# Performance work log

Measured on AMD Instinct MI355X. Metric: run time of the kernel, lower is better.

Reference implementation:

```python
import jax, jax.numpy as jnp
import numpy as np

N_NODES = 20000
N_EDGES = 200000
NODE_DIM = 32
EDGE_DIM = 16
HIDDEN = 32
N_GRAPHS = 64


def setup_inputs() -> dict:
    key = jax.random.key(0)
    ks = jax.random.split(key, 20)
    x = jax.random.normal(ks[0], (N_NODES, NODE_DIM), jnp.float32)
    edge_attr = jax.random.normal(ks[1], (N_EDGES, EDGE_DIM), jnp.float32)
    edge_index = jax.random.randint(ks[2], (2, N_EDGES), 0, N_NODES, jnp.int64)
    batch = jnp.sort(jax.random.randint(ks[3], (N_NODES,), 0, N_GRAPHS, jnp.int64))
    s = 0.1
    # conv1 edge network: EDGE_DIM -> HIDDEN -> NODE_DIM*HIDDEN
    en1_W1 = jax.random.normal(ks[4], (EDGE_DIM, HIDDEN), jnp.float32) * s
    en1_b1 = jnp.zeros((HIDDEN,), jnp.float32)
    en1_W2 = jax.random.normal(ks[5], (HIDDEN, NODE_DIM * HIDDEN), jnp.float32) * s
    en1_b2 = jnp.zeros((NODE_DIM * HIDDEN,), jnp.float32)
    root1 = jax.random.normal(ks[6], (NODE_DIM, HIDDEN), jnp.float32) * s
    bias1 = jnp.zeros((HIDDEN,), jnp.float32)
    # conv2 edge network: EDGE_DIM -> HIDDEN -> HIDDEN*HIDDEN
    en2_W1 = jax.random.normal(ks[7], (EDGE_DIM, HIDDEN), jnp.float32) * s
    en2_b1 = jnp.zeros((HIDDEN,), jnp.float32)
    en2_W2 = jax.random.normal(ks[8], (HIDDEN, HIDDEN * HIDDEN), jnp.float32) * s
    en2_b2 = jnp.zeros((HIDDEN * HIDDEN,), jnp.float32)
    root2 = jax.random.normal(ks[9], (HIDDEN, HIDDEN), jnp.float32) * s
    bias2 = jnp.zeros((HIDDEN,), jnp.float32)
    # output head
    fc_W = jax.random.normal(ks[10], (HIDDEN, 2), jnp.float32) * s
    fc_b = jnp.zeros((2,), jnp.float32)
    return {
        "x": x, "edge_attr": edge_attr, "edge_index": edge_index, "batch": batch,
        "en1_W1": en1_W1, "en1_b1": en1_b1, "en1_W2": en1_W2, "en1_b2": en1_b2,
        "root1": root1, "bias1": bias1,
        "en2_W1": en2_W1, "en2_b1": en2_b1, "en2_W2": en2_W2, "en2_b2": en2_b2,
        "root2": root2, "bias2": bias2,
        "fc_W": fc_W, "fc_b": fc_b,
    }


def _segment_mean(vals, ids, num_segments):
    s = jax.ops.segment_sum(vals, ids, num_segments=num_segments)
    cnt = jax.ops.segment_sum(jnp.ones((vals.shape[0],), vals.dtype), ids, num_segments=num_segments)
    return s / jnp.maximum(cnt, 1.0)[:, None]


def _nnconv(x, src, tgt, edge_attr, W1, b1, W2, b2, root, bias, in_c, out_c, n_nodes):
    # edge MLP -> per-edge weight matrix [E, in_c, out_c]
    h = jax.nn.relu(edge_attr @ W1 + b1)
    Wedge = (h @ W2 + b2).reshape(-1, in_c, out_c)
    # gather source feats, per-edge matvec, scatter-mean to targets
    msg = jnp.einsum('ei,eio->eo', x[src], Wedge)
    agg = _segment_mean(msg, tgt, n_nodes)
    return agg + x @ root + bias


def reference(x, edge_attr, edge_index, batch,
              en1_W1, en1_b1, en1_W2, en1_b2, root1, bias1,
              en2_W1, en2_b1, en2_W2, en2_b2, root2, bias2,
              fc_W, fc_b):
    src, tgt = edge_index[0], edge_index[1]
    h = _nnconv(x, src, tgt, edge_attr, en1_W1, en1_b1, en1_W2, en1_b2,
                root1, bias1, NODE_DIM, HIDDEN, N_NODES)
    h = jax.nn.relu(h)
    h = _nnconv(h, src, tgt, edge_attr, en2_W1, en2_b1, en2_W2, en2_b2,
                root2, bias2, HIDDEN, HIDDEN, N_NODES)
    h = jax.nn.relu(h)
    g = _segment_mean(h, batch, N_GRAPHS)  # global_mean_pool
    return g @ fc_W + fc_b
```

## Files before the change

kernel.cpp:

```cpp
#include <hip/hip_runtime.h>

#define N_NODES   20000
#define N_EDGES   200000
#define NODE_DIM  32
#define EDGE_DIM  16
#define HIDDEN    32
#define N_GRAPHS  64
#define T_NODES   15


__global__ __launch_bounds__(256) void build_deg2_kernel(
    const int* __restrict__ tgts, const int* __restrict__ srcs,
    int* __restrict__ deg_t, int* __restrict__ deg_s)
{
    int e = blockIdx.x * blockDim.x + threadIdx.x;
    if (e >= N_EDGES) return;
    atomicAdd(deg_t + tgts[e], 1);
    atomicAdd(deg_s + srcs[e], 1);
}

__device__ void chunked_scan(const int* __restrict__ deg, int* __restrict__ start,
                             int* __restrict__ cursor, int* partial)
{
    const int C = (N_NODES + 255) / 256;
    int t  = threadIdx.x;
    int lo = t * C;
    int hi = lo + C < N_NODES ? lo + C : N_NODES;
    int s = 0;
    for (int i = lo; i < hi; ++i) s += deg[i];
    partial[t] = s;
    __syncthreads();
    if (t == 0) {
        int run = 0;
        for (int i = 0; i < 256; ++i) { int v = partial[i]; partial[i] = run; run += v; }
    }
    __syncthreads();
    int run = partial[t];
    for (int i = lo; i < hi; ++i) {
        start[i]  = run;
        cursor[i] = run;
        run += deg[i];
    }
    if (lo < N_NODES && hi == N_NODES) start[N_NODES] = run;
    __syncthreads();
}

__global__ __launch_bounds__(256) void scan2_kernel(
    const int* __restrict__ deg_t, int* __restrict__ start_t, int* __restrict__ cur_t,
    const int* __restrict__ deg_s, int* __restrict__ start_s, int* __restrict__ cur_s)
{
    __shared__ int partial[256];
    chunked_scan(deg_t, start_t, cur_t, partial);
    chunked_scan(deg_s, start_s, cur_s, partial);
}

__global__ __launch_bounds__(256) void scatter2_kernel(
    const int* __restrict__ tgts, const int* __restrict__ srcs,
    int* __restrict__ cur_t, int* __restrict__ cur_s,
    int* __restrict__ pos_t, int* __restrict__ eid_s)
{
    int e = blockIdx.x * blockDim.x + threadIdx.x;
    if (e >= N_EDGES) return;
    int p1 = atomicAdd(cur_t + tgts[e], 1);
    pos_t[e] = p1;
    int p2 = atomicAdd(cur_s + srcs[e], 1);
    eid_s[p2] = e;
}

__global__ __launch_bounds__(256, 2) void src_conv_kernel(
    const float* __restrict__ feat,
    const float* __restrict__ ea,
    const int*   __restrict__ srcs,
    const int*   __restrict__ start_s,
    const int*   __restrict__ eid_s,
    const int*   __restrict__ pos_t,
    const float* __restrict__ W1,
    const float* __restrict__ b1,
    const float* __restrict__ W2,
    const float* __restrict__ b2,
    float*       __restrict__ msg)
{
    __shared__ float P[T_NODES][32][32];
    __shared__ float Q[T_NODES][32];
    __shared__ float XT[T_NODES][32];

    int tid = threadIdx.x;
    int v0  = blockIdx.x * T_NODES;
    int T_act = (N_NODES - v0) < T_NODES ? (N_NODES - v0) : T_NODES;

    if (tid < 8 * T_NODES) {
        int t  = tid >> 3;
        int og = tid & 7;
        int vv = v0 + t; if (vv > N_NODES - 1) vv = N_NODES - 1;
        float4 xx = *reinterpret_cast<const float4*>(feat + (size_t)vv * 32 + og * 4);
        *reinterpret_cast<float4*>(&XT[t][og * 4]) = xx;
    }
    __syncthreads();

    {
        int og = tid & 7;
        int k  = tid >> 3;
        float acc[T_NODES][4];
        #pragma unroll
        for (int t = 0; t < T_NODES; ++t) {
            acc[t][0] = 0.f; acc[t][1] = 0.f; acc[t][2] = 0.f; acc[t][3] = 0.f;
        }
        const float* w2p = W2 + (size_t)k * 1024 + og * 4;
        #pragma unroll
        for (int i = 0; i < 32; ++i) {
            float4 w4 = *reinterpret_cast<const float4*>(w2p + i * 32);
            #pragma unroll
            for (int t = 0; t < T_NODES; ++t) {
                float xv = XT[t][i];
                acc[t][0] += xv * w4.x; acc[t][1] += xv * w4.y;
                acc[t][2] += xv * w4.z; acc[t][3] += xv * w4.w;
            }
        }
        #pragma unroll
        for (int t = 0; t < T_NODES; ++t) {
            float4 w; w.x = acc[t][0]; w.y = acc[t][1]; w.z = acc[t][2]; w.w = acc[t][3];
            *reinterpret_cast<float4*>(&P[t][k][og * 4]) = w;
        }
    }
    if (tid < 8 * T_NODES) {
        int t  = tid >> 3;
        int og = tid & 7;
        float q0 = 0.f, q1 = 0.f, q2 = 0.f, q3 = 0.f;
        const float* b2p = b2 + og * 4;
        #pragma unroll
        for (int i = 0; i < 32; ++i) {
            float4 b4 = *reinterpret_cast<const float4*>(b2p + i * 32);
            float xv = XT[t][i];
            q0 += xv * b4.x; q1 += xv * b4.y; q2 += xv * b4.z; q3 += xv * b4.w;
        }
        float4 qq; qq.x = q0; qq.y = q1; qq.z = q2; qq.w = q3;
        *reinterpret_cast<float4*>(&Q[t][og * 4]) = qq;
    }
    __syncthreads();

    int jb = start_s[v0];
    int je = start_s[v0 + T_act];
    int slot = tid >> 5;
    int kl   = tid & 31;
    int half = tid & 32;

    float w1c[EDGE_DIM];
    #pragma unroll
    for (int j = 0; j < EDGE_DIM; ++j) w1c[j] = W1[j * 32 + kl];
    float b1v = b1[kl];

    for (int j0 = jb; j0 < je; j0 += 8) {
        int j = j0 + slot;
        if (j < je) {
            int e  = eid_s[j];
            int sl = srcs[e] - v0;
            int pr = pos_t[e];
            const float4* ea4 = reinterpret_cast<const float4*>(ea + (size_t)e * EDGE_DIM);
            float4 a0 = ea4[0], a1 = ea4[1], a2 = ea4[2], a3 = ea4[3];
            float hv = b1v;
            hv += a0.x * w1c[0]  + a0.y * w1c[1]  + a0.z * w1c[2]  + a0.w * w1c[3];
            hv += a1.x * w1c[4]  + a1.y * w1c[5]  + a1.z * w1c[6]  + a1.w * w1c[7];
            hv += a2.x * w1c[8]  + a2.y * w1c[9]  + a2.z * w1c[10] + a2.w * w1c[11];
            hv += a3.x * w1c[12] + a3.y * w1c[13] + a3.z * w1c[14] + a3.w * w1c[15];
            float h = fmaxf(hv, 0.f);

            float accv = Q[sl][kl];
            #pragma unroll
            for (int k = 0; k < 32; ++k) {
                float hk = __shfl(h, half + k, 64);
                accv += hk * P[sl][k][kl];
            }
            msg[(size_t)pr * 32 + kl] = accv;
        }
    }
}

__global__ __launch_bounds__(256) void gather_update_kernel(
    const float* __restrict__ feat,
    const float* __restrict__ msg,
    const int*   __restrict__ start,
    const float* __restrict__ root,
    const float* __restrict__ bias,
    float*       __restrict__ outf,
    const int*   __restrict__ batch,
    float*       __restrict__ pool,
    float*       __restrict__ pcnt)
{
    int idx = blockIdx.x * blockDim.x + threadIdx.x;
    int v = idx >> 5;
    int o = idx & 31;
    if (v >= N_NODES) return;

    int s0 = start[v], s1 = start[v + 1];
    float sum = 0.0f;
    int j = s0;
    for (; j + 4 <= s1; j += 4) {
        float m0 = msg[(size_t)(j + 0) * 32 + o];
        float m1 = msg[(size_t)(j + 1) * 32 + o];
        float m2 = msg[(size_t)(j + 2) * 32 + o];
        float m3 = msg[(size_t)(j + 3) * 32 + o];
        sum += (m0 + m1) + (m2 + m3);
    }
    for (; j < s1; ++j) sum += msg[(size_t)j * 32 + o];

    int d = s1 - s0;
    float acc = sum / (float)(d > 0 ? d : 1) + bias[o];

    const float* xv = feat + (size_t)v * 32;
    #pragma unroll
    for (int i = 0; i < 32; ++i) acc += xv[i] * root[i * 32 + o];
    acc = fmaxf(acc, 0.0f);

    if (outf) outf[(size_t)v * 32 + o] = acc;
    if (batch) {
        int g = batch[v];
        atomicAdd(pool + (size_t)g * 32 + o, acc);
        if (o == 0) atomicAdd(pcnt + g, 1.0f);
    }
}

__global__ void head_kernel(
    const float* __restrict__ pool, const float* __restrict__ pcnt,
    const float* __restrict__ fcW, const float* __restrict__ fcb,
    float* __restrict__ out)
{
    int g = threadIdx.x;
    if (g >= N_GRAPHS) return;
    float inv = 1.0f / fmaxf(pcnt[g], 1.0f);
    float o0 = fcb[0], o1 = fcb[1];
    #pragma unroll
    for (int i = 0; i < 32; ++i) {
        float m = pool[g * 32 + i] * inv;
        o0 += m * fcW[i * 2 + 0];
        o1 += m * fcW[i * 2 + 1];
    }
    out[g * 2 + 0] = o0;
    out[g * 2 + 1] = o1;
}

__global__ __launch_bounds__(256) void build_deg_kernel(
    const int* __restrict__ tgts, int* __restrict__ deg)
{
    int e = blockIdx.x * blockDim.x + threadIdx.x;
    if (e >= N_EDGES) return;
    atomicAdd(deg + tgts[e], 1);
}

__global__ __launch_bounds__(256) void scan_deg_kernel(
    const int* __restrict__ deg, int* __restrict__ start, int* __restrict__ cursor)
{
    __shared__ int partial[256];
    chunked_scan(deg, start, cursor, partial);
}

__global__ __launch_bounds__(256) void scatter_edges_kernel(
    const int* __restrict__ tgts, int* __restrict__ cursor, int* __restrict__ eid)
{
    int e = blockIdx.x * blockDim.x + threadIdx.x;
    if (e >= N_EDGES) return;
    int pos = atomicAdd(cursor + tgts[e], 1);
    eid[pos] = e;
}

__global__ __launch_bounds__(256) void edge_msg_kernel(
    const float* __restrict__ feat, const float* __restrict__ ea,
    const int* __restrict__ srcs,
    const float* __restrict__ W1, const float* __restrict__ b1,
    const float* __restrict__ W2, const float* __restrict__ b2,
    float* __restrict__ msg)
{
    int e = blockIdx.x * blockDim.x + threadIdx.x;
    if (e >= N_EDGES) return;
    float a[EDGE_DIM];
    const float4* ea4 = reinterpret_cast<const float4*>(ea + (size_t)e * EDGE_DIM);
    #pragma unroll
    for (int q = 0; q < EDGE_DIM / 4; ++q) {
        float4 t = ea4[q];
        a[q*4+0] = t.x; a[q*4+1] = t.y; a[q*4+2] = t.z; a[q*4+3] = t.w;
    }
    int s = srcs[e];
    float x[32];
    const float4* x4 = reinterpret_cast<const float4*>(feat + (size_t)s * 32);
    #pragma unroll
    for (int q = 0; q < 8; ++q) {
        float4 t = x4[q];
        x[q*4+0] = t.x; x[q*4+1] = t.y; x[q*4+2] = t.z; x[q*4+3] = t.w;
    }
    float acc[32];
    #pragma unroll
    for (int o = 0; o < 32; ++o) acc[o] = 0.0f;
    #pragma unroll
    for (int i = 0; i < 32; ++i) {
        float xi = x[i];
        #pragma unroll
        for (int o = 0; o < 32; ++o) acc[o] += xi * b2[i*32+o];
    }
    for (int k = 0; k < 32; ++k) {
        float hk = b1[k];
        #pragma unroll
        for (int j = 0; j < EDGE_DIM; ++j) hk += a[j] * W1[j*32 + k];
        hk = fmaxf(hk, 0.0f);
        const float* w = W2 + (size_t)k * 1024;
        #pragma unroll
        for (int i = 0; i < 32; ++i) {
            float c = hk * x[i];
            #pragma unroll
            for (int o = 0; o < 32; ++o) acc[o] += c * w[i*32+o];
        }
    }
    float4* m4 = reinterpret_cast<float4*>(msg + (size_t)e * 32);
    #pragma unroll
    for (int q = 0; q < 8; ++q) {
        float4 t;
        t.x = acc[q*4+0]; t.y = acc[q*4+1]; t.z = acc[q*4+2]; t.w = acc[q*4+3];
        m4[q] = t;
    }
}

__global__ __launch_bounds__(256) void gather_update_eid_kernel(
    const float* __restrict__ feat, const float* __restrict__ msg,
    const int* __restrict__ start, const int* __restrict__ eid,
    const float* __restrict__ root, const float* __restrict__ bias,
    float* __restrict__ outf, const int* __restrict__ batch,
    float* __restrict__ pool, float* __restrict__ pcnt)
{
    int idx = blockIdx.x * blockDim.x + threadIdx.x;
    int v = idx >> 5;
    int o = idx & 31;
    if (v >= N_NODES) return;
    int s0 = start[v], s1 = start[v + 1];
    float sum = 0.0f;
    for (int j = s0; j < s1; ++j) {
        int e = eid[j];
        sum += msg[(size_t)e * 32 + o];
    }
    int d = s1 - s0;
    float acc = sum / (float)(d > 0 ? d : 1) + bias[o];
    const float* xv = feat + (size_t)v * 32;
    #pragma unroll
    for (int i = 0; i < 32; ++i) acc += xv[i] * root[i * 32 + o];
    acc = fmaxf(acc, 0.0f);
    if (outf) outf[(size_t)v * 32 + o] = acc;
    if (batch) {
        int g = batch[v];
        atomicAdd(pool + (size_t)g * 32 + o, acc);
        if (o == 0) atomicAdd(pcnt + g, 1.0f);
    }
}


extern "C" void kernel_launch(void* const* d_in, const int* in_sizes, int n_in,
                              void* d_out, int out_size, void* d_ws, size_t ws_size,
                              hipStream_t stream)
{
    const float* x      = (const float*)d_in[0];
    const float* ea     = (const float*)d_in[1];
    const int*   ei     = (const int*)d_in[2];
    const int*   batch  = (const int*)d_in[3];
    const float* en1_W1 = (const float*)d_in[4];
    const float* en1_b1 = (const float*)d_in[5];
    const float* en1_W2 = (const float*)d_in[6];
    const float* en1_b2 = (const float*)d_in[7];
    const float* root1  = (const float*)d_in[8];
    const float* bias1  = (const float*)d_in[9];
    const float* en2_W1 = (const float*)d_in[10];
    const float* en2_b1 = (const float*)d_in[11];
    const float* en2_W2 = (const float*)d_in[12];
    const float* en2_b2 = (const float*)d_in[13];
    const float* root2  = (const float*)d_in[14];
    const float* bias2  = (const float*)d_in[15];
    const float* fcW    = (const float*)d_in[16];
    const float* fcb    = (const float*)d_in[17];

    const int* srcs = ei;
    const int* tgts = ei + N_EDGES;

    dim3 eb(256), eg((N_EDGES + 255) / 256);
    dim3 gb(256), gg((N_NODES * 32 + 255) / 256);
    const int NBLK = (N_NODES + T_NODES - 1) / T_NODES;

    size_t need_new = (size_t)2*N_NODES + N_GRAPHS*32 + N_GRAPHS
                    + 2*(N_NODES + 2) + 2*N_NODES + 2*(size_t)N_EDGES
                    + (size_t)N_EDGES*32 + (size_t)N_NODES*32;
    size_t need_old = (size_t)N_NODES + N_GRAPHS*32 + N_GRAPHS
                    + (N_NODES + 1) + N_NODES + N_EDGES
                    + (size_t)N_EDGES*32 + (size_t)N_NODES*32;

    if (ws_size >= need_new * sizeof(float)) {
        int*   deg_t   = (int*)d_ws;
        int*   deg_s   = deg_t + N_NODES;
        float* pool    = (float*)(deg_s + N_NODES);
        float* pcnt    = pool + (size_t)N_GRAPHS*32;
        int*   start_t = (int*)(pcnt + N_GRAPHS);
        int*   cur_t   = start_t + (N_NODES + 2);
        int*   pos_t   = cur_t + N_NODES;
        int*   start_s = pos_t + N_EDGES;
        int*   cur_s   = start_s + (N_NODES + 2);
        int*   eid_s   = cur_s + N_NODES;
        float* msg     = (float*)(eid_s + N_EDGES);
        float* h1      = msg + (size_t)N_EDGES*32;
        size_t zeroBytes = ((size_t)2*N_NODES + N_GRAPHS*32 + N_GRAPHS) * sizeof(float);

        hipMemsetAsync(d_ws, 0, zeroBytes, stream);

        build_deg2_kernel<<<eg, eb, 0, stream>>>(tgts, srcs, deg_t, deg_s);
        scan2_kernel<<<dim3(1), dim3(256), 0, stream>>>(deg_t, start_t, cur_t,
                                                        deg_s, start_s, cur_s);
        scatter2_kernel<<<eg, eb, 0, stream>>>(tgts, srcs, cur_t, cur_s, pos_t, eid_s);

        src_conv_kernel<<<dim3(NBLK), dim3(256), 0, stream>>>(
            x, ea, srcs, start_s, eid_s, pos_t, en1_W1, en1_b1, en1_W2, en1_b2, msg);
        gather_update_kernel<<<gg, gb, 0, stream>>>(x, msg, start_t, root1, bias1,
                                                    h1, nullptr, nullptr, nullptr);
        src_conv_kernel<<<dim3(NBLK), dim3(256), 0, stream>>>(
            h1, ea, srcs, start_s, eid_s, pos_t, en2_W1, en2_b1, en2_W2, en2_b2, msg);
        gather_update_kernel<<<gg, gb, 0, stream>>>(h1, msg, start_t, root2, bias2,
                                                    nullptr, batch, pool, pcnt);

        head_kernel<<<dim3(1), dim3(64), 0, stream>>>(pool, pcnt, fcW, fcb, (float*)d_out);
    } else {
        int*   deg    = (int*)d_ws;
        float* pool   = (float*)(deg + N_NODES);
        float* pcnt   = pool + (size_t)N_GRAPHS*32;
        int*   start  = (int*)(pcnt + N_GRAPHS);
        int*   cursor = start + (N_NODES + 1);
        int*   eid    = cursor + N_NODES;
        float* msg    = (float*)(eid + N_EDGES);
        float* h1     = msg + (size_t)N_EDGES*32;
        size_t zeroBytes = ((size_t)N_NODES + N_GRAPHS*32 + N_GRAPHS) * sizeof(float);

        hipMemsetAsync(d_ws, 0, zeroBytes, stream);

        build_deg_kernel<<<eg, eb, 0, stream>>>(tgts, deg);
        scan_deg_kernel<<<dim3(1), dim3(256), 0, stream>>>(deg, start, cursor);
        scatter_edges_kernel<<<eg, eb, 0, stream>>>(tgts, cursor, eid);

        edge_msg_kernel<<<eg, eb, 0, stream>>>(x, ea, srcs,
                                               en1_W1, en1_b1, en1_W2, en1_b2, msg);
        gather_update_eid_kernel<<<gg, gb, 0, stream>>>(x, msg, start, eid, root1, bias1,
                                                        h1, nullptr, nullptr, nullptr);
        edge_msg_kernel<<<eg, eb, 0, stream>>>(h1, ea, srcs,
                                               en2_W1, en2_b1, en2_W2, en2_b2, msg);
        gather_update_eid_kernel<<<gg, gb, 0, stream>>>(h1, msg, start, eid, root2, bias2,
                                                        nullptr, batch, pool, pcnt);

        head_kernel<<<dim3(1), dim3(64), 0, stream>>>(pool, pcnt, fcW, fcb, (float*)d_out);
    }
}
```

Before: 503.5 us.

## Swizzle shared edge-weight layout and vectorize node gather-update with float4

The per-source-node weight tile P is now stored transposed with an XOR swizzle, and hidden activations are staged in shared memory so each thread reads them with float4 loads instead of 32 cross-lane shuffles. T_NODES drops to 14 to make room in shared memory for the added Hs buffer. gather_update_kernel now handles 8 threads per node with float4 message loads and float4 root/bias reads, in place of 32 scalar threads per node. The fallback path gains a duplicated edge_msg launch, which looks like an accidental edit but only runs when the workspace is too small.

```diff
diff --git a/kernel.cpp b/kernel.cpp
--- a/kernel.cpp
+++ b/kernel.cpp
@@ -6,7 +6,7 @@
 #define EDGE_DIM  16
 #define HIDDEN    32
 #define N_GRAPHS  64
-#define T_NODES   15
+#define T_NODES   14
 
 
 __global__ __launch_bounds__(256) void build_deg2_kernel(
@@ -80,9 +80,10 @@
     const float* __restrict__ b2,
     float*       __restrict__ msg)
 {
-    __shared__ float P[T_NODES][32][32];
-    __shared__ float Q[T_NODES][32];
-    __shared__ float XT[T_NODES][32];
+    __shared__ __align__(16) float P[T_NODES][1024];
+    __shared__ __align__(16) float Q[T_NODES][32];
+    __shared__ __align__(16) float XT[T_NODES][32];
+    __shared__ __align__(16) float Hs[8][32];
 
     int tid = threadIdx.x;
     int v0  = blockIdx.x * T_NODES;
@@ -118,8 +119,11 @@
         }
         #pragma unroll
         for (int t = 0; t < T_NODES; ++t) {
-            float4 w; w.x = acc[t][0]; w.y = acc[t][1]; w.z = acc[t][2]; w.w = acc[t][3];
-            *reinterpret_cast<float4*>(&P[t][k][og * 4]) = w;
+            #pragma unroll
+            for (int c = 0; c < 4; ++c) {
+                int o = og * 4 + c;
+                P[t][o * 32 + (k ^ ((o & 7) << 2))] = acc[t][c];
+            }
         }
     }
     if (tid < 8 * T_NODES) {
@@ -142,7 +146,7 @@
     int je = start_s[v0 + T_act];
     int slot = tid >> 5;
     int kl   = tid & 31;
-    int half = tid & 32;
+    int sw   = (kl & 7) << 2;
 
     float w1c[EDGE_DIM];
     #pragma unroll
@@ -162,20 +166,22 @@
             hv += a1.x * w1c[4]  + a1.y * w1c[5]  + a1.z * w1c[6]  + a1.w * w1c[7];
             hv += a2.x * w1c[8]  + a2.y * w1c[9]  + a2.z * w1c[10] + a2.w * w1c[11];
             hv += a3.x * w1c[12] + a3.y * w1c[13] + a3.z * w1c[14] + a3.w * w1c[15];
-            float h = fmaxf(hv, 0.f);
+            Hs[slot][kl] = fmaxf(hv, 0.f);
 
             float accv = Q[sl][kl];
+            const float* Pt = &P[sl][kl * 32];
             #pragma unroll
-            for (int k = 0; k < 32; ++k) {
-                float hk = __shfl(h, half + k, 64);
-                accv += hk * P[sl][k][kl];
+            for (int kq = 0; kq < 32; kq += 4) {
+                float4 hq = *reinterpret_cast<const float4*>(&Hs[slot][kq]);
+                float4 pq = *reinterpret_cast<const float4*>(&Pt[kq ^ sw]);
+                accv += hq.x * pq.x + hq.y * pq.y + hq.z * pq.z + hq.w * pq.w;
             }
             msg[(size_t)pr * 32 + kl] = accv;
         }
     }
 }
 
-__global__ __launch_bounds__(256) void gather_update_kernel(
+__global__ __launch_bounds__(256, 2) void gather_update_kernel(
     const float* __restrict__ feat,
     const float* __restrict__ msg,
     const int*   __restrict__ start,
@@ -187,35 +193,63 @@
     float*       __restrict__ pcnt)
 {
     int idx = blockIdx.x * blockDim.x + threadIdx.x;
-    int v = idx >> 5;
-    int o = idx & 31;
+    int v  = idx >> 3;
+    int c4 = idx & 7;
     if (v >= N_NODES) return;
 
     int s0 = start[v], s1 = start[v + 1];
-    float sum = 0.0f;
+    const float4* m4 = reinterpret_cast<const float4*>(msg);
+
+    float4 a0 = {0.f,0.f,0.f,0.f}, a1 = {0.f,0.f,0.f,0.f};
+    float4 a2 = {0.f,0.f,0.f,0.f}, a3 = {0.f,0.f,0.f,0.f};
     int j = s0;
     for (; j + 4 <= s1; j += 4) {
-        float m0 = msg[(size_t)(j + 0) * 32 + o];
-        float m1 = msg[(size_t)(j + 1) * 32 + o];
-        float m2 = msg[(size_t)(j + 2) * 32 + o];
-        float m3 = msg[(size_t)(j + 3) * 32 + o];
-        sum += (m0 + m1) + (m2 + m3);
-    }
-    for (; j < s1; ++j) sum += msg[(size_t)j * 32 + o];
+        float4 t0 = m4[(size_t)(j + 0) * 8 + c4];
+        float4 t1 = m4[(size_t)(j + 1) * 8 + c4];
+        float4 t2 = m4[(size_t)(j + 2) * 8 + c4];
+        float4 t3 = m4[(size_t)(j + 3) * 8 + c4];
+        a0.x += t0.x; a0.y += t0.y; a0.z += t0.z; a0.w += t0.w;
+        a1.x += t1.x; a1.y += t1.y; a1.z += t1.z; a1.w += t1.w;
+        a2.x += t2.x; a2.y += t2.y; a2.z += t2.z; a2.w += t2.w;
+        a3.x += t3.x; a3.y += t3.y; a3.z += t3.z; a3.w += t3.w;
+    }
+    for (; j < s1; ++j) {
+        float4 t = m4[(size_t)j * 8 + c4];
+        a0.x += t.x; a0.y += t.y; a0.z += t.z; a0.w += t.w;
+    }
+    float sx = (a0.x + a1.x) + (a2.x + a3.x);
+    float sy = (a0.y + a1.y) + (a2.y + a3.y);
+    float sz = (a0.z + a1.z) + (a2.z + a3.z);
+    float sw_ = (a0.w + a1.w) + (a2.w + a3.w);
 
     int d = s1 - s0;
-    float acc = sum / (float)(d > 0 ? d : 1) + bias[o];
-
-    const float* xv = feat + (size_t)v * 32;
-    #pragma unroll
-    for (int i = 0; i < 32; ++i) acc += xv[i] * root[i * 32 + o];
-    acc = fmaxf(acc, 0.0f);
-
-    if (outf) outf[(size_t)v * 32 + o] = acc;
+    float invd = 1.0f / (float)(d > 0 ? d : 1);
+    float4 bb = *reinterpret_cast<const float4*>(bias + c4 * 4);
+    float ax = sx * invd + bb.x;
+    float ay = sy * invd + bb.y;
+    float az = sz * invd + bb.z;
+    float aw = sw_ * invd + bb.w;
+
+    const float*  xv = feat + (size_t)v * 32;
+    const float4* r4 = reinterpret_cast<const float4*>(root);
+    #pragma unroll
+    for (int i = 0; i < 32; ++i) {
+        float  xi = xv[i];
+        float4 rr = r4[i * 8 + c4];
+        ax += xi * rr.x; ay += xi * rr.y; az += xi * rr.z; aw += xi * rr.w;
+    }
+    ax = fmaxf(ax, 0.f); ay = fmaxf(ay, 0.f); az = fmaxf(az, 0.f); aw = fmaxf(aw, 0.f);
+
+    if (outf) {
+        float4 t; t.x = ax; t.y = ay; t.z = az; t.w = aw;
+        *reinterpret_cast<float4*>(outf + (size_t)v * 32 + c4 * 4) = t;
+    }
     if (batch) {
         int g = batch[v];
-        atomicAdd(pool + (size_t)g * 32 + o, acc);
-        if (o == 0) atomicAdd(pcnt + g, 1.0f);
+        float* p = pool + (size_t)g * 32 + c4 * 4;
+        atomicAdd(p + 0, ax); atomicAdd(p + 1, ay);
+        atomicAdd(p + 2, az); atomicAdd(p + 3, aw);
+        if (c4 == 0) atomicAdd(pcnt + g, 1.0f);
     }
 }
 
@@ -376,14 +410,11 @@
     const int* tgts = ei + N_EDGES;
 
     dim3 eb(256), eg((N_EDGES + 255) / 256);
-    dim3 gb(256), gg((N_NODES * 32 + 255) / 256);
+    dim3 gb(256), gg((N_NODES * 8 + 255) / 256);
     const int NBLK = (N_NODES + T_NODES - 1) / T_NODES;
 
     size_t need_new = (size_t)2*N_NODES + N_GRAPHS*32 + N_GRAPHS
                     + 2*(N_NODES + 2) + 2*N_NODES + 2*(size_t)N_EDGES
-                    + (size_t)N_EDGES*32 + (size_t)N_NODES*32;
-    size_t need_old = (size_t)N_NODES + N_GRAPHS*32 + N_GRAPHS
-                    + (N_NODES + 1) + N_NODES + N_EDGES
                     + (size_t)N_EDGES*32 + (size_t)N_NODES*32;
 
     if (ws_size >= need_new * sizeof(float)) {
@@ -431,19 +462,21 @@
 
         hipMemsetAsync(d_ws, 0, zeroBytes, stream);
 
+        dim3 gg32((N_NODES * 32 + 255) / 256);
         build_deg_kernel<<<eg, eb, 0, stream>>>(tgts, deg);
         scan_deg_kernel<<<dim3(1), dim3(256), 0, stream>>>(deg, start, cursor);
         scatter_edges_kernel<<<eg, eb, 0, stream>>>(tgts, cursor, eid);
 
         edge_msg_kernel<<<eg, eb, 0, stream>>>(x, ea, srcs,
                                                en1_W1, en1_b1, en1_W2, en1_b2, msg);
-        gather_update_eid_kernel<<<gg, gb, 0, stream>>>(x, msg, start, eid, root1, bias1,
-                                                        h1, nullptr, nullptr, nullptr);
+        gather_update_eid_kernel<<<gg32, gb, 0, stream>>>(x, msg, start, eid, root1, bias1,
+                                                          h1, nullptr, nullptr, nullptr);
         edge_msg_kernel<<<eg, eb, 0, stream>>>(h1, ea, srcs,
                                                en2_W1, en2_b1, en2_W2, en2_b2, msg);
-        gather_update_eid_kernel<<<gg, gb, 0, stream>>>(h1, msg, start, eid, root2, bias2,
-                                                        nullptr, batch, pool, pcnt);
-
+        edge_msg_kernel<<<eg, eb, 0, stream>>>(h1, ea, srcs,
+                                               en2_W1, en2_b1, en2_W2, en2_b2, msg);
+        gather_update_eid_kernel<<<gg32, gb, 0, stream>>>(h1, msg, start, eid, root2, bias2,
+                                                          nullptr, batch, pool, pcnt);
         head_kernel<<<dim3(1), dim3(64), 0, stream>>>(pool, pcnt, fcW, fcb, (float*)d_out);
     }
 }
```

Measured after the change: 446.3 us. 11.4% less time.
